# Kernel optimization log

Measured on AMD Instinct MI355X. Metric: run time of the kernel, lower is better.

## Reference

```python
import jax, jax.numpy as jnp
import numpy as np

B, S, D, H = 4, 2048, 1024, 16
HD = D // H
FF = 4 * D
EPS = 1e-5


def setup_inputs() -> dict:
    key = jax.random.key(0)
    ks = jax.random.split(key, 12)
    s = lambda fan_in: 1.0 / np.sqrt(fan_in)
    inp = {
        "x": jax.random.normal(ks[0], (B, S, D), dtype=jnp.float32),
        # attention weights stored as (d_in, d_out)
        "Wq": jax.random.normal(ks[1], (D, D), dtype=jnp.float32) * s(D),
        "Wk": jax.random.normal(ks[2], (D, D), dtype=jnp.float32) * s(D),
        "Wv": jax.random.normal(ks[3], (D, D), dtype=jnp.float32) * s(D),
        "Wo": jax.random.normal(ks[4], (D, D), dtype=jnp.float32) * s(D),
        "bo": jnp.zeros((D,), dtype=jnp.float32),
        # feed-forward
        "W1": jax.random.normal(ks[5], (D, FF), dtype=jnp.float32) * s(D),
        "b1": jnp.zeros((FF,), dtype=jnp.float32),
        "W2": jax.random.normal(ks[6], (FF, D), dtype=jnp.float32) * s(FF),
        "b2": jnp.zeros((D,), dtype=jnp.float32),
        # layernorms
        "g1": jnp.ones((D,), dtype=jnp.float32),
        "be1": jnp.zeros((D,), dtype=jnp.float32),
        "g2": jnp.ones((D,), dtype=jnp.float32),
        "be2": jnp.zeros((D,), dtype=jnp.float32),
    }
    return inp


def _layernorm(x, gamma, beta):
    mean = jnp.mean(x, axis=-1, keepdims=True)
    var = jnp.mean(jnp.square(x - mean), axis=-1, keepdims=True)  # unbiased=False
    return gamma * (x - mean) / jnp.sqrt(var + EPS) + beta


def _gelu_tanh(x):
    c = jnp.sqrt(jnp.asarray(2.0 / jnp.pi, dtype=x.dtype))
    return 0.5 * x * (1.0 + jnp.tanh(c * (x + 0.044715 * x * x * x)))


def _block(x, Wq, Wk, Wv, Wo, bo, W1, b1, W2, b2, g1, be1, g2, be2):
    # --- pre-LN causal multi-head attention ---
    shortcut = x
    h = _layernorm(x, g1, be1)
    q = (h @ Wq).reshape(B, S, H, HD).transpose(0, 2, 1, 3)  # [B,H,S,HD]
    k = (h @ Wk).reshape(B, S, H, HD).transpose(0, 2, 1, 3)
    v = (h @ Wv).reshape(B, S, H, HD).transpose(0, 2, 1, 3)
    scores = jnp.einsum("bhqd,bhkd->bhqk", q, k)
    causal = jnp.tril(jnp.ones((S, S), dtype=bool))  # True = keep
    scores = jnp.where(causal, scores, -jnp.inf)
    attn = jax.nn.softmax(scores / jnp.sqrt(jnp.asarray(HD, scores.dtype)), axis=-1)
    ctx = jnp.einsum("bhqk,bhkd->bqhd", attn, v).reshape(B, S, D)
    x = ctx @ Wo + bo + shortcut
    # --- pre-LN GELU MLP ---
    shortcut = x
    h = _layernorm(x, g2, be2)
    h = _gelu_tanh(h @ W1 + b1) @ W2 + b2
    return h + shortcut


def reference(x, Wq, Wk, Wv, Wo, bo, W1, b1, W2, b2, g1, be1, g2, be2):
    return _block(x, Wq, Wk, Wv, Wo, bo, W1, b1, W2, b2, g1, be1, g2, be2)
```

## Files before the change

### kernel.cpp

```cpp
#include <hip/hip_runtime.h>
#include <cstdint>

#define B_   4
#define S_   2048
#define D_   1024
#define H_   16
#define HD_  64
#define FF_  4096
#define MTOK 8192

typedef short s16x8 __attribute__((ext_vector_type(8), may_alias));
typedef float f32x4 __attribute__((ext_vector_type(4)));
typedef unsigned short u16x4 __attribute__((ext_vector_type(4), may_alias));
typedef unsigned short u16x8 __attribute__((ext_vector_type(8), may_alias));

#define GLD_LDS16(g, l)                                                  \
  __builtin_amdgcn_global_load_lds(                                      \
      (__attribute__((address_space(1))) void*)(g),                      \
      (__attribute__((address_space(3))) void*)(l), 16, 0, 0)

__device__ __forceinline__ unsigned short f2bf(float f) {
  unsigned u = __float_as_uint(f);
  unsigned r = 0x7fffu + ((u >> 16) & 1u);
  return (unsigned short)((u + r) >> 16);
}

__global__ __launch_bounds__(256) void k_transpose(const float* __restrict__ in,
                                                   unsigned short* __restrict__ out,
                                                   int R, int C) {
  __shared__ float tile[32][33];
  int tx = threadIdx.x, ty = threadIdx.y;
  int c0 = blockIdx.x * 32, r0 = blockIdx.y * 32;
#pragma unroll
  for (int j = 0; j < 4; ++j)
    tile[ty + j * 8][tx] = in[(size_t)(r0 + ty + j * 8) * C + (c0 + tx)];
  __syncthreads();
#pragma unroll
  for (int j = 0; j < 4; ++j)
    out[(size_t)(c0 + ty + j * 8) * R + (r0 + tx)] = f2bf(tile[tx][ty + j * 8]);
}

__global__ __launch_bounds__(256) void k_layernorm(const float* __restrict__ x,
                                                   const float* __restrict__ g,
                                                   const float* __restrict__ be,
                                                   unsigned short* __restrict__ out) {
  int row = blockIdx.x, t = threadIdx.x;
  const float4* xr = (const float4*)(x + (size_t)row * D_);
  float4 v = xr[t];
  float s = v.x + v.y + v.z + v.w;
  float q = v.x * v.x + v.y * v.y + v.z * v.z + v.w * v.w;
#pragma unroll
  for (int o = 1; o < 64; o <<= 1) { s += __shfl_xor(s, o); q += __shfl_xor(q, o); }
  __shared__ float red[8];
  int wid = t >> 6;
  if ((t & 63) == 0) { red[wid * 2] = s; red[wid * 2 + 1] = q; }
  __syncthreads();
  s = red[0] + red[2] + red[4] + red[6];
  q = red[1] + red[3] + red[5] + red[7];
  float mean = s * (1.0f / D_);
  float rstd = rsqrtf(q * (1.0f / D_) - mean * mean + 1e-5f);
  float4 gv = ((const float4*)g)[t];
  float4 bv = ((const float4*)be)[t];
  u16x4 o4;
  o4[0] = f2bf(gv.x * (v.x - mean) * rstd + bv.x);
  o4[1] = f2bf(gv.y * (v.y - mean) * rstd + bv.y);
  o4[2] = f2bf(gv.z * (v.z - mean) * rstd + bv.z);
  o4[3] = f2bf(gv.w * (v.w - mean) * rstd + bv.w);
  *(u16x4*)(out + (size_t)row * D_ + t * 4) = o4;
}

template <int MODE, int GN, int GM>
__global__ __launch_bounds__(512, 2) void k_gemmdp(
    const unsigned short* __restrict__ A, const unsigned short* __restrict__ Bt,
    const float* __restrict__ bias, const float* __restrict__ resid,
    unsigned short* __restrict__ outb, float* __restrict__ outf,
    int M, int N, int K) {
  constexpr int BM = 128, BN = 256, BK = 64;
  constexpr int AE = BM * BK;
  constexpr int BE = BN * BK;
  constexpr int BUF_E = AE + BE;
  __shared__ __align__(16) unsigned short smem[3 * BUF_E];
  unsigned short* const Rs = smem;

  const int tid = threadIdx.x;
  const int wid = tid >> 6, lane = tid & 63;
  const int l16 = lane & 15, lg = lane >> 4;
  const int wr = wid >> 2, wc = wid & 3;
  constexpr int GSZ = GN * GM;
  const int nwg = gridDim.x * gridDim.y;
  const int id = blockIdx.y * gridDim.x + blockIdx.x;
  const int chunk = nwg >> 3;
  const int xcd = id & 7, s = id >> 3;
  const int gpx = s / GSZ + xcd * (chunk / GSZ);
  const int r = s % GSZ;
  const int ngx = gridDim.x / GN;
  const int gx = gpx % ngx, gy = gpx / ngx;
  const int n0 = (gx * GN + (r % GN)) * BN;
  const int m0 = (gy * GM + (r / GN)) * BM;

  f32x4 acc[4][4];
#pragma unroll
  for (int m = 0; m < 4; ++m)
#pragma unroll
    for (int n = 0; n < 4; ++n) acc[m][n] = (f32x4)0.0f;

  const unsigned short* aSrc[2]; int aDstB[2];
  const unsigned short* bSrc[4]; int bDstB[4];
#pragma unroll
  for (int g = 0; g < 2; ++g) {
    int q = g * 512 + tid, row = q >> 3, c = q & 7;
    aSrc[g] = A + (size_t)(m0 + row) * K + ((c ^ (row & 7)) << 3);
    aDstB[g] = q * 16;
  }
#pragma unroll
  for (int g = 0; g < 4; ++g) {
    int q = g * 512 + tid, row = q >> 3, c = q & 7;
    bSrc[g] = Bt + (size_t)(n0 + row) * K + ((c ^ (row & 7)) << 3);
    bDstB[g] = q * 16;
  }
  int cSw[2];
  cSw[0] = ((lg) ^ (l16 & 7)) * 8;
  cSw[1] = ((4 + lg) ^ (l16 & 7)) * 8;
  const int aRow = (wr * 64 + l16) * BK;
  const int bRow = (wc * 64 + l16) * BK;

#define STAGE(ti)                                                              \
  {                                                                            \
    const int _b = (ti) % 3;                                                   \
    char* _pa = (char*)(smem + _b * BUF_E);                                    \
    char* _pb = (char*)(smem + _b * BUF_E + AE);                               \
    const int _kt = (ti) * BK;                                                 \
    _Pragma("unroll")                                                          \
    for (int g = 0; g < 2; ++g) GLD_LDS16(aSrc[g] + _kt, _pa + aDstB[g]);      \
    _Pragma("unroll")                                                          \
    for (int g = 0; g < 4; ++g) GLD_LDS16(bSrc[g] + _kt, _pb + bDstB[g]);      \
  }

  const int nt = K / BK;
  STAGE(0); STAGE(1);
  asm volatile("s_waitcnt vmcnt(6)" ::: "memory");
  __builtin_amdgcn_sched_barrier(0);
  __builtin_amdgcn_s_barrier();

  for (int i = 0; i < nt; ++i) {
    if (i + 2 < nt) STAGE(i + 2);
    const unsigned short* pa = smem + (i % 3) * BUF_E + aRow;
    const unsigned short* pb = smem + (i % 3) * BUF_E + AE + bRow;
    s16x8 af[4][2], bfr[4][2];
#pragma unroll
    for (int m = 0; m < 4; ++m) {
      af[m][0] = *(const s16x8*)(pa + m * 16 * BK + cSw[0]);
      af[m][1] = *(const s16x8*)(pa + m * 16 * BK + cSw[1]);
    }
#pragma unroll
    for (int n = 0; n < 4; ++n) {
      bfr[n][0] = *(const s16x8*)(pb + n * 16 * BK + cSw[0]);
      bfr[n][1] = *(const s16x8*)(pb + n * 16 * BK + cSw[1]);
    }
    __builtin_amdgcn_s_setprio(1);
#pragma unroll
    for (int m = 0; m < 4; ++m)
#pragma unroll
      for (int n = 0; n < 4; ++n) {
        acc[m][n] = __builtin_amdgcn_mfma_f32_16x16x32_bf16(af[m][0], bfr[n][0], acc[m][n], 0, 0, 0);
        acc[m][n] = __builtin_amdgcn_mfma_f32_16x16x32_bf16(af[m][1], bfr[n][1], acc[m][n], 0, 0, 0);
      }
    __builtin_amdgcn_s_setprio(0);
    if (i < nt - 2) {
      asm volatile("s_waitcnt vmcnt(6)" ::: "memory");
    } else if (i == nt - 2) {
      asm volatile("s_waitcnt vmcnt(0)" ::: "memory");
    }
    __builtin_amdgcn_sched_barrier(0);
    __builtin_amdgcn_s_barrier();
    __builtin_amdgcn_sched_barrier(0);
  }
#undef STAGE

  if constexpr (MODE == 2) {
#pragma unroll
    for (int n = 0; n < 4; ++n) {
      const int col = n0 + wc * 64 + n * 16 + l16;
      const float bv = bias[col];
#pragma unroll
      for (int m = 0; m < 4; ++m)
#pragma unroll
        for (int r2 = 0; r2 < 4; ++r2) {
          const int row = m0 + wr * 64 + m * 16 + lg * 4 + r2;
          outf[(size_t)row * N + col] = acc[m][n][r2] + bv + resid[(size_t)row * N + col];
        }
    }
    return;
  }

#define ROWMAJOR_FLUSH(DSTPTR, NSTRIDE, COLBASE, XFORM)                        \
  {                                                                            \
    _Pragma("unroll")                                                          \
    for (int p = 0; p < 2; ++p) {                                              \
      if (wr == p) {                                                           \
        _Pragma("unroll")                                                      \
        for (int n = 0; n < 4; ++n) {                                          \
          _Pragma("unroll")                                                    \
          for (int mm = 0; mm < 4; ++mm) {                                     \
            _Pragma("unroll")                                                  \
            for (int r2 = 0; r2 < 4; ++r2) {                                   \
              float xv = acc[mm][n][r2];                                       \
              XFORM;                                                           \
              Rs[(mm * 16 + lg * 4 + r2) * 264 + wc * 64 + n * 16 + l16] = f2bf(xv); \
            }                                                                  \
          }                                                                    \
        }                                                                      \
      }                                                                        \
      __syncthreads();                                                         \
      const int row_l = tid >> 3;                                              \
      _Pragma("unroll")                                                        \
      for (int j = 0; j < 4; ++j) {                                            \
        const int c = (tid & 7) * 4 + j;                                       \
        u16x8 vv = *(const u16x8*)(Rs + row_l * 264 + c * 8);                  \
        *(u16x8*)((DSTPTR) + (size_t)(m0 + p * 64 + row_l) * (NSTRIDE) +       \
                  (COLBASE) + c * 8) = vv;                                     \
      }                                                                        \
      if (p == 0) __syncthreads();                                             \
    }                                                                          \
  }

  if constexpr (MODE == 1) {
    ROWMAJOR_FLUSH(outb, N, n0, {
      xv += bias[n0 + wc * 64 + n * 16 + l16];
      float uu = 0.7978845608028654f * (xv + 0.044715f * xv * xv * xv);
      xv = xv * __builtin_amdgcn_rcpf(1.0f + __builtin_amdgcn_exp2f(uu * -2.885390081777927f));
    });
    return;
  }

  if constexpr (MODE == 3) {
    unsigned short* qout = outb;
    unsigned short* kout = outb + (size_t)MTOK * D_;
    unsigned short* vout = outb + 2 * (size_t)MTOK * D_;
    if (n0 < 1024) {
      ROWMAJOR_FLUSH(qout, D_, n0, { xv *= 0.125f; });
    } else if (n0 < 2048) {
      ROWMAJOR_FLUSH(kout, D_, n0 - 1024, {});
    } else {
      const int vbase = (m0 >> 11) * 1024 + (n0 - 2048);
      const int srow0 = m0 & 2047;
#pragma unroll
      for (int g = 0; g < 4; ++g) {
        if (wc == g) {
#pragma unroll
          for (int n = 0; n < 4; ++n)
#pragma unroll
            for (int m = 0; m < 4; ++m) {
              u16x4 pk;
#pragma unroll
              for (int r2 = 0; r2 < 4; ++r2) pk[r2] = f2bf(acc[m][n][r2]);
              *(u16x4*)(Rs + (n * 16 + l16) * 264 + wr * 64 + m * 16 + lg * 4) = pk;
            }
        }
        __syncthreads();
        const int row_l = tid >> 3;
#pragma unroll
        for (int j = 0; j < 2; ++j) {
          const int c = (tid & 7) * 2 + j;
          u16x8 vv = *(const u16x8*)(Rs + row_l * 264 + c * 8);
          *(u16x8*)(vout + (size_t)(vbase + g * 64 + row_l) * S_ + srow0 + c * 8) = vv;
        }
        if (g < 3) __syncthreads();
      }
    }
    return;
  }
#undef ROWMAJOR_FLUSH
}

__global__ __launch_bounds__(256, 3) void k_attn(
    const unsigned short* __restrict__ qg, const unsigned short* __restrict__ kg,
    const unsigned short* __restrict__ vtg, unsigned short* __restrict__ ctx) {
  const int id = blockIdx.x;
  const int bh = (id & 7) + 8 * (id >> 7);
  const int p  = (id >> 3) & 15;
  const int qtA = p, qtB = 31 - p;
  const int tid = threadIdx.x, wid = tid >> 6, lane = tid & 63;
  const int l16 = lane & 15, lg = lane >> 4;
  __shared__ __align__(16) unsigned short Ks[2][64 * 64];
  __shared__ __align__(16) unsigned short Vs[2][64 * 64];
  __shared__ __align__(16) unsigned short Ps[4][2][16 * 72];

  const size_t headoff = (size_t)(bh >> 4) * ((size_t)S_ * D_) + (size_t)(bh & 15) * HD_;
  const unsigned short* Kb = kg + headoff;
  const unsigned short* Vt = vtg + (size_t)bh * ((size_t)HD_ * S_);

  const int qrowA = qtA * 64 + wid * 16 + l16;
  const int qrowB = qtB * 64 + wid * 16 + l16;
  s16x8 qfA0 = *(const s16x8*)(qg + headoff + (size_t)qrowA * D_ + lg * 8);
  s16x8 qfA1 = *(const s16x8*)(qg + headoff + (size_t)qrowA * D_ + 32 + lg * 8);
  s16x8 qfB0 = *(const s16x8*)(qg + headoff + (size_t)qrowB * D_ + lg * 8);
  s16x8 qfB1 = *(const s16x8*)(qg + headoff + (size_t)qrowB * D_ + 32 + lg * 8);

  f32x4 oA[4], oB[4];
#pragma unroll
  for (int n = 0; n < 4; ++n) { oA[n] = (f32x4)0.0f; oB[n] = (f32x4)0.0f; }
  float lsumA[4] = {0.f, 0.f, 0.f, 0.f};
  float lsumB[4] = {0.f, 0.f, 0.f, 0.f};
  unsigned short* psA = &Ps[wid][0][0];
  unsigned short* psB = &Ps[wid][1][0];
  const int myrowA = qtA * 64 + wid * 16 + lg * 4;
  const int myrowB = qtB * 64 + wid * 16 + lg * 4;
  const float L2E = 1.4426950408889634f;

  const unsigned short* kSrc[2];
  const unsigned short* vSrc[2];
  int dstOff[2];
#pragma unroll
  for (int i = 0; i < 2; ++i) {
    int chunk = (i * 4 + wid) * 64 + lane;
    int row = chunk >> 3, pc = chunk & 7;
    int scol = (pc ^ (row & 7)) * 8;
    kSrc[i] = Kb + (size_t)row * D_ + scol;
    vSrc[i] = Vt + (size_t)row * S_ + scol;
    dstOff[i] = (i * 4 + wid) * 1024;
  }

#pragma unroll
  for (int i = 0; i < 2; ++i) {
    GLD_LDS16(kSrc[i], (char*)Ks[0] + dstOff[i]);
    GLD_LDS16(vSrc[i], (char*)Vs[0] + dstOff[i]);
  }
  __syncthreads();

  for (int t = 0; t <= qtB; ++t) {
    const int cur = t & 1;
    const int kv0 = t * 64;
    const bool doA = (t <= qtA);
    if (t < qtB) {
      const int kvn = kv0 + 64;
#pragma unroll
      for (int i = 0; i < 2; ++i) {
        GLD_LDS16(kSrc[i] + (size_t)kvn * D_, (char*)Ks[cur ^ 1] + dstOff[i]);
        GLD_LDS16(vSrc[i] + kvn, (char*)Vs[cur ^ 1] + dstOff[i]);
      }
    }
    const unsigned short* Kc = Ks[cur];
    const unsigned short* Vc = Vs[cur];
    s16x8 kf0[4], kf1[4];
#pragma unroll
    for (int n = 0; n < 4; ++n) {
      int srow = n * 16 + l16, sw = srow & 7;
      kf0[n] = *(const s16x8*)(Kc + srow * 64 + (lg ^ sw) * 8);
      kf1[n] = *(const s16x8*)(Kc + srow * 64 + ((4 + lg) ^ sw) * 8);
    }
    f32x4 saA[4], saB[4];
    if (doA) {
#pragma unroll
      for (int n = 0; n < 4; ++n) {
        saA[n] = (f32x4)0.0f;
        saA[n] = __builtin_amdgcn_mfma_f32_16x16x32_bf16(qfA0, kf0[n], saA[n], 0, 0, 0);
        saA[n] = __builtin_amdgcn_mfma_f32_16x16x32_bf16(qfA1, kf1[n], saA[n], 0, 0, 0);
      }
    }
#pragma unroll
    for (int n = 0; n < 4; ++n) {
      saB[n] = (f32x4)0.0f;
      saB[n] = __builtin_amdgcn_mfma_f32_16x16x32_bf16(qfB0, kf0[n], saB[n], 0, 0, 0);
      saB[n] = __builtin_amdgcn_mfma_f32_16x16x32_bf16(qfB1, kf1[n], saB[n], 0, 0, 0);
    }
    if (doA) {
      const bool mask = (t == qtA);
#pragma unroll
      for (int r = 0; r < 4; ++r)
#pragma unroll
        for (int n = 0; n < 4; ++n) {
          float pv = exp2f((saA[n][r] - 12.0f) * L2E);
          if (mask && (kv0 + n * 16 + l16) > (myrowA + r)) pv = 0.0f;
          lsumA[r] += pv;
          psA[(lg * 4 + r) * 72 + n * 16 + l16] = f2bf(pv);
        }
    }
    {
      const bool mask = (t == qtB);
#pragma unroll
      for (int r = 0; r < 4; ++r)
#pragma unroll
        for (int n = 0; n < 4; ++n) {
          float pv = exp2f((saB[n][r] - 12.0f) * L2E);
          if (mask && (kv0 + n * 16 + l16) > (myrowB + r)) pv = 0.0f;
          lsumB[r] += pv;
          psB[(lg * 4 + r) * 72 + n * 16 + l16] = f2bf(pv);
        }
    }
    s16x8 vf0[4], vf1[4];
#pragma unroll
    for (int n = 0; n < 4; ++n) {
      int srow = n * 16 + l16, sw = srow & 7;
      vf0[n] = *(const s16x8*)(Vc + srow * 64 + (lg ^ sw) * 8);
      vf1[n] = *(const s16x8*)(Vc + srow * 64 + ((4 + lg) ^ sw) * 8);
    }
    __builtin_amdgcn_sched_barrier(0);
    asm volatile("s_waitcnt lgkmcnt(0)" ::: "memory");
    __builtin_amdgcn_sched_barrier(0);
    {
      s16x8 paB0 = *(const s16x8*)(psB + l16 * 72 + lg * 8);
      s16x8 paB1 = *(const s16x8*)(psB + l16 * 72 + 32 + lg * 8);
#pragma unroll
      for (int n = 0; n < 4; ++n) {
        oB[n] = __builtin_amdgcn_mfma_f32_16x16x32_bf16(paB0, vf0[n], oB[n], 0, 0, 0);
        oB[n] = __builtin_amdgcn_mfma_f32_16x16x32_bf16(paB1, vf1[n], oB[n], 0, 0, 0);
      }
      if (doA) {
        s16x8 paA0 = *(const s16x8*)(psA + l16 * 72 + lg * 8);
        s16x8 paA1 = *(const s16x8*)(psA + l16 * 72 + 32 + lg * 8);
#pragma unroll
        for (int n = 0; n < 4; ++n) {
          oA[n] = __builtin_amdgcn_mfma_f32_16x16x32_bf16(paA0, vf0[n], oA[n], 0, 0, 0);
          oA[n] = __builtin_amdgcn_mfma_f32_16x16x32_bf16(paA1, vf1[n], oA[n], 0, 0, 0);
        }
      }
    }
    __syncthreads();
  }

#pragma unroll
  for (int r = 0; r < 4; ++r) {
    float la = lsumA[r], lb = lsumB[r];
    la += __shfl_xor(la, 1); lb += __shfl_xor(lb, 1);
    la += __shfl_xor(la, 2); lb += __shfl_xor(lb, 2);
    la += __shfl_xor(la, 4); lb += __shfl_xor(lb, 4);
    la += __shfl_xor(la, 8); lb += __shfl_xor(lb, 8);
    float ia = 1.0f / la, ib = 1.0f / lb;
#pragma unroll
    for (int n = 0; n < 4; ++n) {
      ctx[headoff + (size_t)(myrowA + r) * D_ + n * 16 + l16] = f2bf(oA[n][r] * ia);
      ctx[headoff + (size_t)(myrowB + r) * D_ + n * 16 + l16] = f2bf(oB[n][r] * ib);
    }
  }
}

extern "C" void kernel_launch(void* const* d_in, const int* in_sizes, int n_in,
                              void* d_out, int out_size, void* d_ws, size_t ws_size,
                              hipStream_t stream) {
  (void)in_sizes; (void)n_in; (void)out_size; (void)ws_size;
  const float* x   = (const float*)d_in[0];
  const float* Wq  = (const float*)d_in[1];
  const float* Wk  = (const float*)d_in[2];
  const float* Wv  = (const float*)d_in[3];
  const float* Wo  = (const float*)d_in[4];
  const float* bo  = (const float*)d_in[5];
  const float* W1  = (const float*)d_in[6];
  const float* b1  = (const float*)d_in[7];
  const float* W2  = (const float*)d_in[8];
  const float* b2  = (const float*)d_in[9];
  const float* g1  = (const float*)d_in[10];
  const float* be1 = (const float*)d_in[11];
  const float* g2  = (const float*)d_in[12];
  const float* be2 = (const float*)d_in[13];
  float* out = (float*)d_out;

  char* w = (char*)d_ws;
  const size_t MB = 1ull << 20;
  unsigned short* wqkvT = (unsigned short*)(w + 0 * MB);
  unsigned short* woT   = (unsigned short*)(w + 6 * MB);
  unsigned short* w1T   = (unsigned short*)(w + 8 * MB);
  unsigned short* w2T   = (unsigned short*)(w + 16 * MB);
  unsigned short* hb    = (unsigned short*)(w + 24 * MB);
  float*          x2    = (float*)(w + 40 * MB);
  unsigned short* qkv   = (unsigned short*)(w + 72 * MB);
  unsigned short* qb    = qkv;
  unsigned short* kb    = qkv + (size_t)MTOK * D_;
  unsigned short* vbT   = qkv + 2 * (size_t)MTOK * D_;
  unsigned short* cxb   = (unsigned short*)(w + 120 * MB);
  unsigned short* act   = (unsigned short*)(w + 72 * MB);

  dim3 tb(32, 8);
  k_transpose<<<dim3(32, 32), tb, 0, stream>>>(Wq, wqkvT, 1024, 1024);
  k_transpose<<<dim3(32, 32), tb, 0, stream>>>(Wk, wqkvT + 1024 * 1024, 1024, 1024);
  k_transpose<<<dim3(32, 32), tb, 0, stream>>>(Wv, wqkvT + 2048 * 1024, 1024, 1024);
  k_transpose<<<dim3(32, 32), tb, 0, stream>>>(Wo, woT, 1024, 1024);
  k_transpose<<<dim3(128, 32), tb, 0, stream>>>(W1, w1T, 1024, 4096);
  k_transpose<<<dim3(32, 128), tb, 0, stream>>>(W2, w2T, 4096, 1024);

  k_layernorm<<<MTOK, 256, 0, stream>>>(x, g1, be1, hb);

  k_gemmdp<3, 4, 8><<<dim3(12, 64), 512, 0, stream>>>(hb, wqkvT, nullptr, nullptr, qkv, nullptr, MTOK, 3072, 1024);

  k_attn<<<1024, 256, 0, stream>>>(qb, kb, vbT, cxb);

  k_gemmdp<2, 4, 8><<<dim3(4, 64), 512, 0, stream>>>(cxb, woT, bo, x, nullptr, x2, MTOK, 1024, 1024);

  k_layernorm<<<MTOK, 256, 0, stream>>>(x2, g2, be2, hb);

  k_gemmdp<1, 4, 8><<<dim3(16, 64), 512, 0, stream>>>(hb, w1T, b1, nullptr, act, nullptr, MTOK, 4096, 1024);
  k_gemmdp<2, 1, 32><<<dim3(4, 64), 512, 0, stream>>>(act, w2T, b2, x2, nullptr, out, MTOK, 1024, 4096);
}
```

Measured before the change: 428.6 us.

## Replace direct global-to-LDS triple buffering with register-staged double buffering in GEMM

The GEMM main loop switches from three LDS buffers filled by asynchronous global_load_lds to two LDS buffers filled through registers. The next K tile is read into VGPRs while the current tile is computed, then written to LDS with the XOR swizzle applied on the write side. This cuts LDS use from three tile buffers to two and replaces the explicit vmcnt waits with plain __syncthreads. In exchange it adds 48 staging VGPRs and extra LDS write instructions, and prefetch depth drops from two tiles ahead to one, so latency hiding may get worse.

```diff
diff --git a/kernel.cpp b/kernel.cpp
--- a/kernel.cpp
+++ b/kernel.cpp
@@ -79,7 +79,7 @@
   constexpr int AE = BM * BK;
   constexpr int BE = BN * BK;
   constexpr int BUF_E = AE + BE;
-  __shared__ __align__(16) unsigned short smem[3 * BUF_E];
+  __shared__ __align__(16) unsigned short smem[2 * BUF_E];
   unsigned short* const Rs = smem;
 
   const int tid = threadIdx.x;
@@ -104,19 +104,19 @@
 #pragma unroll
     for (int n = 0; n < 4; ++n) acc[m][n] = (f32x4)0.0f;
 
-  const unsigned short* aSrc[2]; int aDstB[2];
-  const unsigned short* bSrc[4]; int bDstB[4];
+  const unsigned short* aSrcL[2]; int aWOff[2];
+  const unsigned short* bSrcL[4]; int bWOff[4];
 #pragma unroll
   for (int g = 0; g < 2; ++g) {
     int q = g * 512 + tid, row = q >> 3, c = q & 7;
-    aSrc[g] = A + (size_t)(m0 + row) * K + ((c ^ (row & 7)) << 3);
-    aDstB[g] = q * 16;
+    aSrcL[g] = A + (size_t)(m0 + row) * K + c * 8;
+    aWOff[g] = row * BK + ((c ^ (row & 7)) << 3);
   }
 #pragma unroll
   for (int g = 0; g < 4; ++g) {
     int q = g * 512 + tid, row = q >> 3, c = q & 7;
-    bSrc[g] = Bt + (size_t)(n0 + row) * K + ((c ^ (row & 7)) << 3);
-    bDstB[g] = q * 16;
+    bSrcL[g] = Bt + (size_t)(n0 + row) * K + c * 8;
+    bWOff[g] = row * BK + ((c ^ (row & 7)) << 3);
   }
   int cSw[2];
   cSw[0] = ((lg) ^ (l16 & 7)) * 8;
@@ -124,58 +124,71 @@
   const int aRow = (wr * 64 + l16) * BK;
   const int bRow = (wc * 64 + l16) * BK;
 
-#define STAGE(ti)                                                              \
+#define LOADG(R, ti)                                                           \
   {                                                                            \
-    const int _b = (ti) % 3;                                                   \
-    char* _pa = (char*)(smem + _b * BUF_E);                                    \
-    char* _pb = (char*)(smem + _b * BUF_E + AE);                               \
     const int _kt = (ti) * BK;                                                 \
     _Pragma("unroll")                                                          \
-    for (int g = 0; g < 2; ++g) GLD_LDS16(aSrc[g] + _kt, _pa + aDstB[g]);      \
-    _Pragma("unroll")                                                          \
-    for (int g = 0; g < 4; ++g) GLD_LDS16(bSrc[g] + _kt, _pb + bDstB[g]);      \
+    for (int g = 0; g < 2; ++g) R[g] = *(const u16x8*)(aSrcL[g] + _kt);        \
+    _Pragma("unroll")                                                          \
+    for (int g = 0; g < 4; ++g) R[2 + g] = *(const u16x8*)(bSrcL[g] + _kt);    \
+  }
+#define DSWRITE(R, BUF)                                                        \
+  {                                                                            \
+    unsigned short* _pa = smem + (BUF) * BUF_E;                                \
+    unsigned short* _pb = _pa + AE;                                            \
+    _Pragma("unroll")                                                          \
+    for (int g = 0; g < 2; ++g) *(u16x8*)(_pa + aWOff[g]) = R[g];              \
+    _Pragma("unroll")                                                          \
+    for (int g = 0; g < 4; ++g) *(u16x8*)(_pb + bWOff[g]) = R[2 + g];          \
+  }
+#define COMPUTE(BUF)                                                           \
+  {                                                                            \
+    const unsigned short* pa = smem + (BUF) * BUF_E + aRow;                    \
+    const unsigned short* pb = smem + (BUF) * BUF_E + AE + bRow;               \
+    s16x8 af[4][2], bfr[4][2];                                                 \
+    _Pragma("unroll")                                                          \
+    for (int m = 0; m < 4; ++m) {                                              \
+      af[m][0] = *(const s16x8*)(pa + m * 16 * BK + cSw[0]);                   \
+      af[m][1] = *(const s16x8*)(pa + m * 16 * BK + cSw[1]);                   \
+    }                                                                          \
+    _Pragma("unroll")                                                          \
+    for (int n = 0; n < 4; ++n) {                                              \
+      bfr[n][0] = *(const s16x8*)(pb + n * 16 * BK + cSw[0]);                  \
+      bfr[n][1] = *(const s16x8*)(pb + n * 16 * BK + cSw[1]);                  \
+    }                                                                          \
+    __builtin_amdgcn_s_setprio(1);                                             \
+    _Pragma("unroll")                                                          \
+    for (int m = 0; m < 4; ++m)                                                \
+      _Pragma("unroll")                                                        \
+      for (int n = 0; n < 4; ++n) {                                            \
+        acc[m][n] = __builtin_amdgcn_mfma_f32_16x16x32_bf16(af[m][0], bfr[n][0], acc[m][n], 0, 0, 0); \
+        acc[m][n] = __builtin_amdgcn_mfma_f32_16x16x32_bf16(af[m][1], bfr[n][1], acc[m][n], 0, 0, 0); \
+      }                                                                        \
+    __builtin_amdgcn_s_setprio(0);                                             \
   }
 
   const int nt = K / BK;
-  STAGE(0); STAGE(1);
-  asm volatile("s_waitcnt vmcnt(6)" ::: "memory");
-  __builtin_amdgcn_sched_barrier(0);
-  __builtin_amdgcn_s_barrier();
-
-  for (int i = 0; i < nt; ++i) {
-    if (i + 2 < nt) STAGE(i + 2);
-    const unsigned short* pa = smem + (i % 3) * BUF_E + aRow;
-    const unsigned short* pb = smem + (i % 3) * BUF_E + AE + bRow;
-    s16x8 af[4][2], bfr[4][2];
-#pragma unroll
-    for (int m = 0; m < 4; ++m) {
-      af[m][0] = *(const s16x8*)(pa + m * 16 * BK + cSw[0]);
-      af[m][1] = *(const s16x8*)(pa + m * 16 * BK + cSw[1]);
-    }
-#pragma unroll
-    for (int n = 0; n < 4; ++n) {
-      bfr[n][0] = *(const s16x8*)(pb + n * 16 * BK + cSw[0]);
-      bfr[n][1] = *(const s16x8*)(pb + n * 16 * BK + cSw[1]);
-    }
-    __builtin_amdgcn_s_setprio(1);
-#pragma unroll
-    for (int m = 0; m < 4; ++m)
-#pragma unroll
-      for (int n = 0; n < 4; ++n) {
-        acc[m][n] = __builtin_amdgcn_mfma_f32_16x16x32_bf16(af[m][0], bfr[n][0], acc[m][n], 0, 0, 0);
-        acc[m][n] = __builtin_amdgcn_mfma_f32_16x16x32_bf16(af[m][1], bfr[n][1], acc[m][n], 0, 0, 0);
-      }
-    __builtin_amdgcn_s_setprio(0);
-    if (i < nt - 2) {
-      asm volatile("s_waitcnt vmcnt(6)" ::: "memory");
-    } else if (i == nt - 2) {
-      asm volatile("s_waitcnt vmcnt(0)" ::: "memory");
-    }
-    __builtin_amdgcn_sched_barrier(0);
-    __builtin_amdgcn_s_barrier();
-    __builtin_amdgcn_sched_barrier(0);
-  }
-#undef STAGE
+  u16x8 rA[6], rB[6];
+  LOADG(rA, 0)
+  DSWRITE(rA, 0)
+  __syncthreads();
+  LOADG(rB, 1)
+
+  for (int i = 0; i < nt; i += 2) {
+    if (i + 2 < nt) LOADG(rA, i + 2)
+    COMPUTE(0)
+    DSWRITE(rB, 1)
+    __syncthreads();
+    if (i + 3 < nt) LOADG(rB, i + 3)
+    COMPUTE(1)
+    if (i + 2 < nt) {
+      DSWRITE(rA, 0)
+      __syncthreads();
+    }
+  }
+#undef LOADG
+#undef DSWRITE
+#undef COMPUTE
 
   if constexpr (MODE == 2) {
 #pragma unroll
@@ -193,6 +206,7 @@
     return;
   }
 
+  __syncthreads();
 #define ROWMAJOR_FLUSH(DSTPTR, NSTRIDE, COLBASE, XFORM)                        \
   {                                                                            \
     _Pragma("unroll")                                                          \
```

New measurement: 435.1 us. Within noise of the previous version (+1.5%).
